# Optimization experiments

Measured on AMD Instinct MI355X. Metric: run time of the kernel, lower is better.

The kernel has to match this reference:

```python
import jax, jax.numpy as jnp
import numpy as np
import math

HEADS = 16
D_MODEL = 1024
D_K = D_MODEL // HEADS


def setup_inputs() -> dict:
    key = jax.random.key(0)
    ks = jax.random.split(key, 11)
    B, S = 2, 2048
    s = 1.0 / math.sqrt(D_MODEL)
    return {
        "q": jax.random.normal(ks[0], (B, S, D_MODEL), jnp.float32),
        "k": jax.random.normal(ks[1], (B, S, D_MODEL), jnp.float32),
        "v": jax.random.normal(ks[2], (B, S, D_MODEL), jnp.float32),
        "Wq": jax.random.normal(ks[3], (D_MODEL, D_MODEL), jnp.float32) * s,
        "bq": jax.random.normal(ks[4], (D_MODEL,), jnp.float32) * s,
        "Wk": jax.random.normal(ks[5], (D_MODEL, D_MODEL), jnp.float32) * s,
        "bk": jax.random.normal(ks[6], (D_MODEL,), jnp.float32) * s,
        "Wv": jax.random.normal(ks[7], (D_MODEL, D_MODEL), jnp.float32) * s,
        "bv": jax.random.normal(ks[8], (D_MODEL,), jnp.float32) * s,
        "Wo": jax.random.normal(ks[9], (D_MODEL, D_MODEL), jnp.float32) * s,
        "bo": jax.random.normal(ks[10], (D_MODEL,), jnp.float32) * s,
    }


def reference(q, k, v, Wq, bq, Wk, bk, Wv, bv, Wo, bo):
    B, S, _ = q.shape
    # linear projections, split heads: [B, H, S, d_k]
    def proj(x, W, b):
        y = x @ W.T + b
        return y.reshape(B, -1, HEADS, D_K).transpose(0, 2, 1, 3)
    qh, kh, vh = proj(q, Wq, bq), proj(k, Wk, bk), proj(v, Wv, bv)
    # abs-modified scaled dot-product attention (no mask, eval -> no dropout)
    scores = jnp.abs(jnp.einsum("bhsd,bhtd->bhst", qh, kh) / math.sqrt(D_K))
    attn = jax.nn.softmax(scores, axis=-1)
    out = jnp.einsum("bhst,bhtd->bhsd", attn, vh)
    concat = out.transpose(0, 2, 1, 3).reshape(B, S, D_MODEL)
    return concat @ Wo.T + bo
```

## Files before the change

### kernel.cpp

```cpp
#include <hip/hip_runtime.h>

#define HEADS 16
#define DK 64
#define DM 1024
#define SEQ 2048
#define BATCH 2

using bf16x8 = __attribute__((ext_vector_type(8))) short;
using short4v = __attribute__((ext_vector_type(4))) short;
using f32x4 = __attribute__((ext_vector_type(4))) float;

static __device__ __forceinline__ short f2bf(float x) {
  union { float f; unsigned u; } c;
  c.f = x;
  unsigned r = (c.u + 0x7FFFu + ((c.u >> 16) & 1u)) >> 16;
  return (short)r;
}

static __device__ __forceinline__ unsigned pk2bf(float lo, float hi) {
#if __has_builtin(__builtin_amdgcn_cvt_pk_bf16_f32)
  auto t = __builtin_amdgcn_cvt_pk_bf16_f32(lo, hi);
  if constexpr (sizeof(t) == 4) {
    unsigned u;
    __builtin_memcpy(&u, &t, 4);
    return u;
  } else {
    return (unsigned)(unsigned short)f2bf(lo) |
           ((unsigned)(unsigned short)f2bf(hi) << 16);
  }
#else
  return (unsigned)(unsigned short)f2bf(lo) |
         ((unsigned)(unsigned short)f2bf(hi) << 16);
#endif
}

static __device__ __forceinline__ void gload_lds16(const void* g, void* l) {
  __builtin_amdgcn_global_load_lds(
      (const __attribute__((address_space(1))) void*)g,
      (__attribute__((address_space(3))) void*)l, 16, 0, 0);
}

__global__ __launch_bounds__(256) void cvt7(
    const float* __restrict__ s0, const float* __restrict__ s1,
    const float* __restrict__ s2, const float* __restrict__ s3,
    const float* __restrict__ s4, const float* __restrict__ s5,
    const float* __restrict__ s6, short* d0, short* d1, short* d2, short* d3,
    short* d4, short* d5, short* d6) {
  const int y = blockIdx.y;
  const float* s;
  short* d;
  int n;
  switch (y) {
    case 0: s = s0; d = d0; n = BATCH * SEQ * DM; break;
    case 1: s = s1; d = d1; n = BATCH * SEQ * DM; break;
    case 2: s = s2; d = d2; n = BATCH * SEQ * DM; break;
    case 3: s = s3; d = d3; n = DM * DM; break;
    case 4: s = s4; d = d4; n = DM * DM; break;
    case 5: s = s5; d = d5; n = DM * DM; break;
    default: s = s6; d = d6; n = DM * DM; break;
  }
  const int n4 = n >> 2;
  const int stride = gridDim.x * 256;
  for (int i = blockIdx.x * 256 + threadIdx.x; i < n4; i += stride) {
    float4 v = ((const float4*)s)[i];
    uint2 o;
    o.x = pk2bf(v.x, v.y);
    o.y = pk2bf(v.z, v.w);
    ((uint2*)d)[i] = o;
  }
}

__global__ __launch_bounds__(256) void proj_qkv(
    const short* __restrict__ Aq, const short* __restrict__ Ak,
    const short* __restrict__ Av, const short* __restrict__ Wq_,
    const short* __restrict__ Wk_, const short* __restrict__ Wv_,
    const float* __restrict__ bq, const float* __restrict__ bk,
    const float* __restrict__ bv, short* __restrict__ Qh,
    short* __restrict__ Kh, short* __restrict__ Vt) {
  __shared__ short smem[128 * 136];
  short* As = smem;
  short* Ws = smem + 8192;

  const int z = blockIdx.z;
  const short* A = z == 0 ? Aq : z == 1 ? Ak : Av;
  const short* W = z == 0 ? Wq_ : z == 1 ? Wk_ : Wv_;
  const float* bias = z == 0 ? bq : z == 1 ? bk : bv;
  short* C = z == 0 ? Qh : z == 1 ? Kh : Vt;
  const bool tr = (z == 2);

  const int tid = threadIdx.x;
  const int wave = tid >> 6, lane = tid & 63;
  const int quad = lane >> 4, l15 = lane & 15;
  const int n0 = blockIdx.x * 128, m0 = blockIdx.y * 128;
  const int mh = (wave & 1) * 64, nh = (wave >> 1) * 64;
  const int ldr = lane >> 3, ldc = lane & 7;

  f32x4 acc[4][4] = {};

  for (int k0 = 0; k0 < 1024; k0 += 64) {
    __syncthreads();
#pragma unroll
    for (int i = 0; i < 8; ++i) {
      int seg = wave * 8 + i;
      int r = (seg & 15) * 8 + ldr;
      int kb = ldc ^ (r & 7);
      if (seg < 16)
        gload_lds16(&A[(size_t)(m0 + r) * 1024 + k0 + kb * 8], &As[seg * 512]);
      else
        gload_lds16(&W[(size_t)(n0 + r) * 1024 + k0 + kb * 8],
                    &Ws[(seg - 16) * 512]);
    }
    __syncthreads();
#pragma unroll
    for (int ks = 0; ks < 2; ++ks) {
      bf16x8 a[4], b[4];
      int kb = ks * 4 + quad;
#pragma unroll
      for (int f = 0; f < 4; ++f) {
        int rm = mh + f * 16 + l15;
        int rn = nh + f * 16 + l15;
        a[f] = *(const bf16x8*)&As[rm * 64 + (kb ^ (rm & 7)) * 8];
        b[f] = *(const bf16x8*)&Ws[rn * 64 + (kb ^ (rn & 7)) * 8];
      }
#pragma unroll
      for (int mf = 0; mf < 4; ++mf)
#pragma unroll
        for (int nf = 0; nf < 4; ++nf)
          acc[mf][nf] = __builtin_amdgcn_mfma_f32_16x16x32_bf16(
              a[mf], b[nf], acc[mf][nf], 0, 0, 0);
    }
  }

  float bvv[4];
#pragma unroll
  for (int nf = 0; nf < 4; ++nf) bvv[nf] = bias[n0 + nh + nf * 16 + l15];

  __syncthreads();
  short* Cb = smem;

  if (!tr) {
#pragma unroll
    for (int mf = 0; mf < 4; ++mf)
#pragma unroll
      for (int r = 0; r < 4; ++r) {
        int row = mh + mf * 16 + quad * 4 + r;
        unsigned u01 =
            pk2bf(acc[mf][0][r] + bvv[0], acc[mf][1][r] + bvv[1]);
        unsigned u23 =
            pk2bf(acc[mf][2][r] + bvv[2], acc[mf][3][r] + bvv[3]);
        Cb[row * 136 + nh + l15] = (short)u01;
        Cb[row * 136 + nh + 16 + l15] = (short)(u01 >> 16);
        Cb[row * 136 + nh + 32 + l15] = (short)u23;
        Cb[row * 136 + nh + 48 + l15] = (short)(u23 >> 16);
      }
    __syncthreads();
#pragma unroll
    for (int j = 0; j < 8; ++j) {
      int cid = tid + 256 * j;
      int row = cid >> 4, cb = cid & 15;
      bf16x8 v = *(const bf16x8*)&Cb[row * 136 + cb * 8];
      int m = m0 + row, n = n0 + cb * 8;
      int b = m >> 11, s = m & (SEQ - 1), h = n >> 6, d = n & 63;
      *(bf16x8*)&C[((size_t)(b * HEADS + h) * SEQ + s) * DK + d] = v;
    }
  } else {
#pragma unroll
    for (int mf = 0; mf < 4; ++mf)
#pragma unroll
      for (int nf = 0; nf < 4; ++nf) {
        unsigned u01 =
            pk2bf(acc[mf][nf][0] + bvv[nf], acc[mf][nf][1] + bvv[nf]);
        unsigned u23 =
            pk2bf(acc[mf][nf][2] + bvv[nf], acc[mf][nf][3] + bvv[nf]);
        int base_ = (nh + nf * 16 + l15) * 136 + mh + mf * 16 + quad * 4;
        *(unsigned*)&Cb[base_] = u01;
        *(unsigned*)&Cb[base_ + 2] = u23;
      }
    __syncthreads();
#pragma unroll
    for (int j = 0; j < 8; ++j) {
      int cid = tid + 256 * j;
      int row = cid >> 4, cb = cid & 15;
      bf16x8 v = *(const bf16x8*)&Cb[row * 136 + cb * 8];
      int n = n0 + row, m = m0 + cb * 8;
      int b = m >> 11, s = m & (SEQ - 1), h = n >> 6, d = n & 63;
      *(bf16x8*)&C[((size_t)(b * HEADS + h) * DK + d) * SEQ + s] = v;
    }
  }
}

__global__ __launch_bounds__(256) void proj_out(const short* __restrict__ A,
                                                const short* __restrict__ W,
                                                const float* __restrict__ bias,
                                                float* __restrict__ C) {
  __shared__ short smem[12288];
  short* As = smem;
  short* Ws = smem + 8192;

  const int tid = threadIdx.x;
  const int wave = tid >> 6, lane = tid & 63;
  const int quad = lane >> 4, l15 = lane & 15;
  const int n0 = blockIdx.x * 64, m0 = blockIdx.y * 128;
  const int mh = (wave & 1) * 64, nh = (wave >> 1) * 32;
  const int ldr = lane >> 3, ldc = lane & 7;

  f32x4 acc[4][2] = {};

  for (int k0 = 0; k0 < 1024; k0 += 64) {
    __syncthreads();
#pragma unroll
    for (int i = 0; i < 6; ++i) {
      int seg = wave * 6 + i;
      if (seg < 16) {
        int r = seg * 8 + ldr;
        int kb = ldc ^ (r & 7);
        gload_lds16(&A[(size_t)(m0 + r) * 1024 + k0 + kb * 8], &As[seg * 512]);
      } else {
        int r = (seg - 16) * 8 + ldr;
        int kb = ldc ^ (r & 7);
        gload_lds16(&W[(size_t)(n0 + r) * 1024 + k0 + kb * 8],
                    &Ws[(seg - 16) * 512]);
      }
    }
    __syncthreads();
#pragma unroll
    for (int ks = 0; ks < 2; ++ks) {
      bf16x8 a[4], b[2];
      int kb = ks * 4 + quad;
#pragma unroll
      for (int f = 0; f < 4; ++f) {
        int rm = mh + f * 16 + l15;
        a[f] = *(const bf16x8*)&As[rm * 64 + (kb ^ (rm & 7)) * 8];
      }
#pragma unroll
      for (int f = 0; f < 2; ++f) {
        int rn = nh + f * 16 + l15;
        b[f] = *(const bf16x8*)&Ws[rn * 64 + (kb ^ (rn & 7)) * 8];
      }
#pragma unroll
      for (int mf = 0; mf < 4; ++mf)
#pragma unroll
        for (int nf = 0; nf < 2; ++nf)
          acc[mf][nf] = __builtin_amdgcn_mfma_f32_16x16x32_bf16(
              a[mf], b[nf], acc[mf][nf], 0, 0, 0);
    }
  }

  float bvv[2];
#pragma unroll
  for (int nf = 0; nf < 2; ++nf) bvv[nf] = bias[n0 + nh + nf * 16 + l15];
#pragma unroll
  for (int mf = 0; mf < 4; ++mf)
#pragma unroll
    for (int nf = 0; nf < 2; ++nf)
#pragma unroll
      for (int r = 0; r < 4; ++r)
        C[(size_t)(m0 + mh + mf * 16 + quad * 4 + r) * 1024 + n0 + nh +
          nf * 16 + l15] = acc[mf][nf][r] + bvv[nf];
}

__global__ __launch_bounds__(128) void attn_mfma(const short* __restrict__ Qh,
                                                 const short* __restrict__ Kh,
                                                 const short* __restrict__ VtG,
                                                 short* __restrict__ concat) {
  __shared__ short Ks[2][64 * 64];
  __shared__ short Vt[2][64 * 64];
  __shared__ short Ps[64 * 64];

  const int tid = threadIdx.x;
  const int wave = tid >> 6, lane = tid & 63;
  const int quad = lane >> 4, l15 = lane & 15;
  const int bh = blockIdx.y;
  const int q0 = blockIdx.x * 64;
  const size_t base = (size_t)bh * SEQ * DK;
  const int ldr = lane >> 3, ldc = lane & 7;

  bf16x8 qf[2][2];
#pragma unroll
  for (int mf = 0; mf < 2; ++mf)
#pragma unroll
    for (int ks = 0; ks < 2; ++ks)
      qf[mf][ks] =
          *(const bf16x8*)&Qh[base +
                              (size_t)(q0 + wave * 32 + mf * 16 + l15) * 64 +
                              ks * 32 + quad * 8];

  f32x4 O[2][4] = {};
  float lsum[2][4] = {};

#define STAGE_TILE(kt_, buf_)                                              \
  {                                                                        \
    _Pragma("unroll") for (int i_ = 0; i_ < 4; ++i_) {                     \
      int seg = wave * 4 + i_;                                             \
      int row = seg * 8 + ldr;                                             \
      int kb = ldc ^ (row & 7);                                            \
      int key = 2 * (row & 15) + ((row >> 4) & 1) + 32 * (row >> 5);       \
      gload_lds16(&Kh[base + (size_t)((kt_)*64 + key) * 64 + kb * 8],      \
                  &Ks[buf_][seg * 512]);                                   \
      gload_lds16(&VtG[base + (size_t)row * SEQ + (kt_)*64 + kb * 8],      \
                  &Vt[buf_][seg * 512]);                                   \
    }                                                                      \
  }

  STAGE_TILE(0, 0);

  const float CE = 0.18033688011112042f;

  for (int kt = 0; kt < SEQ / 64; ++kt) {
    const int cur = kt & 1;
    __syncthreads();
    if (kt + 1 < SEQ / 64) STAGE_TILE(kt + 1, cur ^ 1);

    f32x4 sf[2][4] = {};
#pragma unroll
    for (int ks = 0; ks < 2; ++ks) {
      bf16x8 bfr[4];
      int kb = ks * 4 + quad;
#pragma unroll
      for (int nf = 0; nf < 4; ++nf) {
        int n = nf * 16 + l15;
        bfr[nf] = *(const bf16x8*)&Ks[cur][n * 64 + (kb ^ (n & 7)) * 8];
      }
#pragma unroll
      for (int mf = 0; mf < 2; ++mf)
#pragma unroll
        for (int nf = 0; nf < 4; ++nf)
          sf[mf][nf] = __builtin_amdgcn_mfma_f32_16x16x32_bf16(
              qf[mf][ks], bfr[nf], sf[mf][nf], 0, 0, 0);
    }

#pragma unroll
    for (int mf = 0; mf < 2; ++mf)
#pragma unroll
      for (int r = 0; r < 4; ++r) {
        float e0 = exp2f(fabsf(sf[mf][0][r]) * CE);
        float e1 = exp2f(fabsf(sf[mf][1][r]) * CE);
        float e2 = exp2f(fabsf(sf[mf][2][r]) * CE);
        float e3 = exp2f(fabsf(sf[mf][3][r]) * CE);
        lsum[mf][r] += (e0 + e1) + (e2 + e3);
        unsigned u01 = pk2bf(e0, e1);
        unsigned u23 = pk2bf(e2, e3);
        int row = wave * 32 + mf * 16 + quad * 4 + r;
        int sw = (row >> 1) & 7;
        int off = (2 * l15) & 7;
        short* rp = &Ps[row * 64];
        *(unsigned*)&rp[(((l15 >> 2) ^ sw) << 3) + off] = u01;
        *(unsigned*)&rp[(((4 + (l15 >> 2)) ^ sw) << 3) + off] = u23;
      }
    __threadfence_block();

#pragma unroll
    for (int ks = 0; ks < 2; ++ks) {
      bf16x8 av[2], bvv[4];
      int kb = ks * 4 + quad;
#pragma unroll
      for (int mf = 0; mf < 2; ++mf) {
        int row = wave * 32 + mf * 16 + l15;
        av[mf] =
            *(const bf16x8*)&Ps[row * 64 + ((kb ^ ((row >> 1) & 7)) << 3)];
      }
#pragma unroll
      for (int nf = 0; nf < 4; ++nf) {
        int n = nf * 16 + l15;
        bvv[nf] = *(const bf16x8*)&Vt[cur][n * 64 + (kb ^ (n & 7)) * 8];
      }
#pragma unroll
      for (int mf = 0; mf < 2; ++mf)
#pragma unroll
        for (int nf = 0; nf < 4; ++nf)
          O[mf][nf] = __builtin_amdgcn_mfma_f32_16x16x32_bf16(
              av[mf], bvv[nf], O[mf][nf], 0, 0, 0);
    }
  }

  float inv[2][4];
#pragma unroll
  for (int mf = 0; mf < 2; ++mf)
#pragma unroll
    for (int r = 0; r < 4; ++r) {
      float s = lsum[mf][r];
#pragma unroll
      for (int x = 1; x < 16; x <<= 1) s += __shfl_xor(s, x, 64);
      inv[mf][r] = 1.f / s;
    }

  __syncthreads();
#pragma unroll
  for (int mf = 0; mf < 2; ++mf)
#pragma unroll
    for (int r = 0; r < 4; ++r) {
      unsigned u01 =
          pk2bf(O[mf][0][r] * inv[mf][r], O[mf][1][r] * inv[mf][r]);
      unsigned u23 =
          pk2bf(O[mf][2][r] * inv[mf][r], O[mf][3][r] * inv[mf][r]);
      int row = wave * 32 + mf * 16 + quad * 4 + r;
      int sw = (row >> 1) & 7;
      short* rp = &Ps[row * 64];
      rp[((((l15) >> 3) ^ sw) << 3) + (l15 & 7)] = (short)u01;
      rp[((((16 + l15) >> 3) ^ sw) << 3) + (l15 & 7)] = (short)(u01 >> 16);
      rp[((((32 + l15) >> 3) ^ sw) << 3) + (l15 & 7)] = (short)u23;
      rp[((((48 + l15) >> 3) ^ sw) << 3) + (l15 & 7)] = (short)(u23 >> 16);
    }
  __syncthreads();
  const int b = bh >> 4, h = bh & 15;
#pragma unroll
  for (int j = 0; j < 4; ++j) {
    int cid = tid + 128 * j;
    int row = cid >> 3, cb = cid & 7;
    bf16x8 v = *(const bf16x8*)&Ps[row * 64 + ((cb ^ ((row >> 1) & 7)) << 3)];
    *(bf16x8*)&concat[((size_t)(b * SEQ + q0 + row)) * DM + h * 64 + cb * 8] =
        v;
  }
#undef STAGE_TILE
}

extern "C" void kernel_launch(void* const* d_in, const int* in_sizes, int n_in,
                              void* d_out, int out_size, void* d_ws,
                              size_t ws_size, hipStream_t stream) {
  const float* q = (const float*)d_in[0];
  const float* k = (const float*)d_in[1];
  const float* v = (const float*)d_in[2];
  const float* Wq = (const float*)d_in[3];
  const float* bq = (const float*)d_in[4];
  const float* Wk = (const float*)d_in[5];
  const float* bk = (const float*)d_in[6];
  const float* Wv = (const float*)d_in[7];
  const float* bv = (const float*)d_in[8];
  const float* Wo = (const float*)d_in[9];
  const float* bo = (const float*)d_in[10];

  short* ws = (short*)d_ws;
  const size_t T4 = (size_t)BATCH * SEQ * DM;
  const size_t T1 = (size_t)DM * DM;
  short* qb = ws;
  short* kb_ = ws + T4;
  short* vb = ws + 2 * T4;
  short* Wqb = ws + 3 * T4;
  short* Wkb = Wqb + T1;
  short* Wvb = Wqb + 2 * T1;
  short* Wob = Wqb + 3 * T1;
  short* Qh = Wqb + 4 * T1;
  short* Kh = Qh + T4;
  short* VtG = Qh + 2 * T4;
  short* cc = Qh + 3 * T4;

  cvt7<<<dim3(1024, 7), 256, 0, stream>>>(q, k, v, Wq, Wk, Wv, Wo, qb, kb_, vb,
                                          Wqb, Wkb, Wvb, Wob);

  proj_qkv<<<dim3(DM / 128, (BATCH * SEQ) / 128, 3), 256, 0, stream>>>(
      qb, kb_, vb, Wqb, Wkb, Wvb, bq, bk, bv, Qh, Kh, VtG);

  attn_mfma<<<dim3(SEQ / 64, BATCH * HEADS), 128, 0, stream>>>(Qh, Kh, VtG,
                                                               cc);

  proj_out<<<dim3(DM / 64, (BATCH * SEQ) / 128), 256, 0, stream>>>(
      cc, Wob, bo, (float*)d_out);
}
```

Before: 266.7 us.

## Split attention block into four 16-row waves and drop K/V double buffering

```diff
diff --git a/kernel.cpp b/kernel.cpp
--- a/kernel.cpp
+++ b/kernel.cpp
@@ -259,12 +259,12 @@
           nf * 16 + l15] = acc[mf][nf][r] + bvv[nf];
 }
 
-__global__ __launch_bounds__(128) void attn_mfma(const short* __restrict__ Qh,
+__global__ __launch_bounds__(256) void attn_mfma(const short* __restrict__ Qh,
                                                  const short* __restrict__ Kh,
                                                  const short* __restrict__ VtG,
                                                  short* __restrict__ concat) {
-  __shared__ short Ks[2][64 * 64];
-  __shared__ short Vt[2][64 * 64];
+  __shared__ short Ks[64 * 64];
+  __shared__ short Vt[64 * 64];
   __shared__ short Ps[64 * 64];
 
   const int tid = threadIdx.x;
@@ -275,43 +275,32 @@
   const size_t base = (size_t)bh * SEQ * DK;
   const int ldr = lane >> 3, ldc = lane & 7;
 
-  bf16x8 qf[2][2];
-#pragma unroll
-  for (int mf = 0; mf < 2; ++mf)
-#pragma unroll
-    for (int ks = 0; ks < 2; ++ks)
-      qf[mf][ks] =
-          *(const bf16x8*)&Qh[base +
-                              (size_t)(q0 + wave * 32 + mf * 16 + l15) * 64 +
-                              ks * 32 + quad * 8];
-
-  f32x4 O[2][4] = {};
-  float lsum[2][4] = {};
-
-#define STAGE_TILE(kt_, buf_)                                              \
-  {                                                                        \
-    _Pragma("unroll") for (int i_ = 0; i_ < 4; ++i_) {                     \
-      int seg = wave * 4 + i_;                                             \
-      int row = seg * 8 + ldr;                                             \
-      int kb = ldc ^ (row & 7);                                            \
-      int key = 2 * (row & 15) + ((row >> 4) & 1) + 32 * (row >> 5);       \
-      gload_lds16(&Kh[base + (size_t)((kt_)*64 + key) * 64 + kb * 8],      \
-                  &Ks[buf_][seg * 512]);                                   \
-      gload_lds16(&VtG[base + (size_t)row * SEQ + (kt_)*64 + kb * 8],      \
-                  &Vt[buf_][seg * 512]);                                   \
-    }                                                                      \
-  }
-
-  STAGE_TILE(0, 0);
+  bf16x8 qf[2];
+#pragma unroll
+  for (int ks = 0; ks < 2; ++ks)
+    qf[ks] = *(const bf16x8*)&Qh[base + (size_t)(q0 + wave * 16 + l15) * 64 +
+                                 ks * 32 + quad * 8];
+
+  f32x4 O[4] = {};
+  float lsum[4] = {};
 
   const float CE = 0.18033688011112042f;
 
   for (int kt = 0; kt < SEQ / 64; ++kt) {
-    const int cur = kt & 1;
-    __syncthreads();
-    if (kt + 1 < SEQ / 64) STAGE_TILE(kt + 1, cur ^ 1);
-
-    f32x4 sf[2][4] = {};
+    __syncthreads();
+#pragma unroll
+    for (int i = 0; i < 2; ++i) {
+      int seg = wave * 2 + i;
+      int row = seg * 8 + ldr;
+      int kb = ldc ^ (row & 7);
+      gload_lds16(&Kh[base + (size_t)(kt * 64 + row) * 64 + kb * 8],
+                  &Ks[seg * 512]);
+      gload_lds16(&VtG[base + (size_t)row * SEQ + kt * 64 + kb * 8],
+                  &Vt[seg * 512]);
+    }
+    __syncthreads();
+
+    f32x4 sf[4] = {};
 #pragma unroll
     for (int ks = 0; ks < 2; ++ks) {
       bf16x8 bfr[4];
@@ -319,99 +308,85 @@
 #pragma unroll
       for (int nf = 0; nf < 4; ++nf) {
         int n = nf * 16 + l15;
-        bfr[nf] = *(const bf16x8*)&Ks[cur][n * 64 + (kb ^ (n & 7)) * 8];
-      }
-#pragma unroll
-      for (int mf = 0; mf < 2; ++mf)
-#pragma unroll
-        for (int nf = 0; nf < 4; ++nf)
-          sf[mf][nf] = __builtin_amdgcn_mfma_f32_16x16x32_bf16(
-              qf[mf][ks], bfr[nf], sf[mf][nf], 0, 0, 0);
-    }
-
-#pragma unroll
-    for (int mf = 0; mf < 2; ++mf)
-#pragma unroll
-      for (int r = 0; r < 4; ++r) {
-        float e0 = exp2f(fabsf(sf[mf][0][r]) * CE);
-        float e1 = exp2f(fabsf(sf[mf][1][r]) * CE);
-        float e2 = exp2f(fabsf(sf[mf][2][r]) * CE);
-        float e3 = exp2f(fabsf(sf[mf][3][r]) * CE);
-        lsum[mf][r] += (e0 + e1) + (e2 + e3);
-        unsigned u01 = pk2bf(e0, e1);
-        unsigned u23 = pk2bf(e2, e3);
-        int row = wave * 32 + mf * 16 + quad * 4 + r;
-        int sw = (row >> 1) & 7;
-        int off = (2 * l15) & 7;
-        short* rp = &Ps[row * 64];
-        *(unsigned*)&rp[(((l15 >> 2) ^ sw) << 3) + off] = u01;
-        *(unsigned*)&rp[(((4 + (l15 >> 2)) ^ sw) << 3) + off] = u23;
-      }
+        bfr[nf] = *(const bf16x8*)&Ks[n * 64 + (kb ^ (n & 7)) * 8];
+      }
+#pragma unroll
+      for (int nf = 0; nf < 4; ++nf)
+        sf[nf] = __builtin_amdgcn_mfma_f32_16x16x32_bf16(qf[ks], bfr[nf],
+                                                         sf[nf], 0, 0, 0);
+    }
+
+    const int h2 = l15 >> 3, lo3 = l15 & 7;
+#pragma unroll
+    for (int r = 0; r < 4; ++r) {
+      float e0 = exp2f(fabsf(sf[0][r]) * CE);
+      float e1 = exp2f(fabsf(sf[1][r]) * CE);
+      float e2 = exp2f(fabsf(sf[2][r]) * CE);
+      float e3 = exp2f(fabsf(sf[3][r]) * CE);
+      lsum[r] += (e0 + e1) + (e2 + e3);
+      unsigned u01 = pk2bf(e0, e1);
+      unsigned u23 = pk2bf(e2, e3);
+      int row = wave * 16 + quad * 4 + r;
+      int sw = (row >> 1) & 7;
+      short* rp = &Ps[row * 64];
+      rp[(((0 + h2) ^ sw) << 3) + lo3] = (short)u01;
+      rp[(((2 + h2) ^ sw) << 3) + lo3] = (short)(u01 >> 16);
+      rp[(((4 + h2) ^ sw) << 3) + lo3] = (short)u23;
+      rp[(((6 + h2) ^ sw) << 3) + lo3] = (short)(u23 >> 16);
+    }
     __threadfence_block();
 
 #pragma unroll
     for (int ks = 0; ks < 2; ++ks) {
-      bf16x8 av[2], bvv[4];
+      bf16x8 av, bvv[4];
       int kb = ks * 4 + quad;
-#pragma unroll
-      for (int mf = 0; mf < 2; ++mf) {
-        int row = wave * 32 + mf * 16 + l15;
-        av[mf] =
-            *(const bf16x8*)&Ps[row * 64 + ((kb ^ ((row >> 1) & 7)) << 3)];
-      }
+      int row = wave * 16 + l15;
+      av = *(const bf16x8*)&Ps[row * 64 + ((kb ^ ((row >> 1) & 7)) << 3)];
 #pragma unroll
       for (int nf = 0; nf < 4; ++nf) {
         int n = nf * 16 + l15;
-        bvv[nf] = *(const bf16x8*)&Vt[cur][n * 64 + (kb ^ (n & 7)) * 8];
-      }
-#pragma unroll
-      for (int mf = 0; mf < 2; ++mf)
-#pragma unroll
-        for (int nf = 0; nf < 4; ++nf)
-          O[mf][nf] = __builtin_amdgcn_mfma_f32_16x16x32_bf16(
-              av[mf], bvv[nf], O[mf][nf], 0, 0, 0);
-    }
-  }
-
-  float inv[2][4];
-#pragma unroll
-  for (int mf = 0; mf < 2; ++mf)
-#pragma unroll
-    for (int r = 0; r < 4; ++r) {
-      float s = lsum[mf][r];
-#pragma unroll
-      for (int x = 1; x < 16; x <<= 1) s += __shfl_xor(s, x, 64);
-      inv[mf][r] = 1.f / s;
-    }
+        bvv[nf] = *(const bf16x8*)&Vt[n * 64 + (kb ^ (n & 7)) * 8];
+      }
+#pragma unroll
+      for (int nf = 0; nf < 4; ++nf)
+        O[nf] = __builtin_amdgcn_mfma_f32_16x16x32_bf16(av, bvv[nf], O[nf], 0,
+                                                        0, 0);
+    }
+  }
+
+  float inv[4];
+#pragma unroll
+  for (int r = 0; r < 4; ++r) {
+    float s = lsum[r];
+#pragma unroll
+    for (int x = 1; x < 16; x <<= 1) s += __shfl_xor(s, x, 64);
+    inv[r] = 1.f / s;
+  }
 
   __syncthreads();
-#pragma unroll
-  for (int mf = 0; mf < 2; ++mf)
-#pragma unroll
-    for (int r = 0; r < 4; ++r) {
-      unsigned u01 =
-          pk2bf(O[mf][0][r] * inv[mf][r], O[mf][1][r] * inv[mf][r]);
-      unsigned u23 =
-          pk2bf(O[mf][2][r] * inv[mf][r], O[mf][3][r] * inv[mf][r]);
-      int row = wave * 32 + mf * 16 + quad * 4 + r;
-      int sw = (row >> 1) & 7;
-      short* rp = &Ps[row * 64];
-      rp[((((l15) >> 3) ^ sw) << 3) + (l15 & 7)] = (short)u01;
-      rp[((((16 + l15) >> 3) ^ sw) << 3) + (l15 & 7)] = (short)(u01 >> 16);
-      rp[((((32 + l15) >> 3) ^ sw) << 3) + (l15 & 7)] = (short)u23;
-      rp[((((48 + l15) >> 3) ^ sw) << 3) + (l15 & 7)] = (short)(u23 >> 16);
-    }
+  const int h2 = l15 >> 3, lo3 = l15 & 7;
+#pragma unroll
+  for (int r = 0; r < 4; ++r) {
+    unsigned u01 = pk2bf(O[0][r] * inv[r], O[1][r] * inv[r]);
+    unsigned u23 = pk2bf(O[2][r] * inv[r], O[3][r] * inv[r]);
+    int row = wave * 16 + quad * 4 + r;
+    int sw = (row >> 1) & 7;
+    short* rp = &Ps[row * 64];
+    rp[(((0 + h2) ^ sw) << 3) + lo3] = (short)u01;
+    rp[(((2 + h2) ^ sw) << 3) + lo3] = (short)(u01 >> 16);
+    rp[(((4 + h2) ^ sw) << 3) + lo3] = (short)u23;
+    rp[(((6 + h2) ^ sw) << 3) + lo3] = (short)(u23 >> 16);
+  }
   __syncthreads();
   const int b = bh >> 4, h = bh & 15;
 #pragma unroll
-  for (int j = 0; j < 4; ++j) {
-    int cid = tid + 128 * j;
+  for (int j = 0; j < 2; ++j) {
+    int cid = tid + 256 * j;
     int row = cid >> 3, cb = cid & 7;
     bf16x8 v = *(const bf16x8*)&Ps[row * 64 + ((cb ^ ((row >> 1) & 7)) << 3)];
     *(bf16x8*)&concat[((size_t)(b * SEQ + q0 + row)) * DM + h * 64 + cb * 8] =
         v;
   }
-#undef STAGE_TILE
 }
 
 extern "C" void kernel_launch(void* const* d_in, const int* in_sizes, int n_in,
@@ -450,7 +425,7 @@
   proj_qkv<<<dim3(DM / 128, (BATCH * SEQ) / 128, 3), 256, 0, stream>>>(
       qb, kb_, vb, Wqb, Wkb, Wvb, bq, bk, bv, Qh, Kh, VtG);
 
-  attn_mfma<<<dim3(SEQ / 64, BATCH * HEADS), 128, 0, stream>>>(Qh, Kh, VtG,
+  attn_mfma<<<dim3(SEQ / 64, BATCH * HEADS), 256, 0, stream>>>(Qh, Kh, VtG,
                                                                cc);
 
   proj_out<<<dim3(DM / 64, (BATCH * SEQ) / 128), 256, 0, stream>>>(
```

Result: faster. 254.8 us (-4.4%).

## Double query rows per attention block and reorder V-transpose/P layouts

Applied to the files above, without the earlier changes.

```diff
diff --git a/kernel.cpp b/kernel.cpp
--- a/kernel.cpp
+++ b/kernel.cpp
@@ -167,15 +167,13 @@
 #pragma unroll
     for (int mf = 0; mf < 4; ++mf)
 #pragma unroll
-      for (int nf = 0; nf < 4; ++nf) {
-        unsigned u01 =
-            pk2bf(acc[mf][nf][0] + bvv[nf], acc[mf][nf][1] + bvv[nf]);
-        unsigned u23 =
-            pk2bf(acc[mf][nf][2] + bvv[nf], acc[mf][nf][3] + bvv[nf]);
-        int base_ = (nh + nf * 16 + l15) * 136 + mh + mf * 16 + quad * 4;
-        *(unsigned*)&Cb[base_] = u01;
-        *(unsigned*)&Cb[base_ + 2] = u23;
-      }
+      for (int nf = 0; nf < 4; ++nf)
+#pragma unroll
+        for (int j = 0; j < 4; ++j) {
+          int slot = 16 * quad + 4 * j + mf;
+          Cb[(nh + nf * 16 + l15) * 136 + mh + slot] =
+              f2bf(acc[mf][nf][j] + bvv[nf]);
+        }
     __syncthreads();
 #pragma unroll
     for (int j = 0; j < 8; ++j) {
@@ -259,59 +257,57 @@
           nf * 16 + l15] = acc[mf][nf][r] + bvv[nf];
 }
 
-__global__ __launch_bounds__(128) void attn_mfma(const short* __restrict__ Qh,
-                                                 const short* __restrict__ Kh,
-                                                 const short* __restrict__ VtG,
-                                                 short* __restrict__ concat) {
+__global__ __launch_bounds__(128, 1) void attn_mfma(
+    const short* __restrict__ Qh, const short* __restrict__ Kh,
+    const short* __restrict__ VtG, short* __restrict__ concat) {
   __shared__ short Ks[2][64 * 64];
   __shared__ short Vt[2][64 * 64];
-  __shared__ short Ps[64 * 64];
+  __shared__ short Ps[128 * 64];
 
   const int tid = threadIdx.x;
   const int wave = tid >> 6, lane = tid & 63;
   const int quad = lane >> 4, l15 = lane & 15;
   const int bh = blockIdx.y;
-  const int q0 = blockIdx.x * 64;
+  const int q0 = blockIdx.x * 128;
   const size_t base = (size_t)bh * SEQ * DK;
   const int ldr = lane >> 3, ldc = lane & 7;
 
-  bf16x8 qf[2][2];
-#pragma unroll
-  for (int mf = 0; mf < 2; ++mf)
+  bf16x8 qf[4][2];
+#pragma unroll
+  for (int mf = 0; mf < 4; ++mf)
 #pragma unroll
     for (int ks = 0; ks < 2; ++ks)
       qf[mf][ks] =
           *(const bf16x8*)&Qh[base +
-                              (size_t)(q0 + wave * 32 + mf * 16 + l15) * 64 +
+                              (size_t)(q0 + wave * 64 + mf * 16 + l15) * 64 +
                               ks * 32 + quad * 8];
 
-  f32x4 O[2][4] = {};
-  float lsum[2][4] = {};
-
-#define STAGE_TILE(kt_, buf_)                                              \
-  {                                                                        \
-    _Pragma("unroll") for (int i_ = 0; i_ < 4; ++i_) {                     \
-      int seg = wave * 4 + i_;                                             \
-      int row = seg * 8 + ldr;                                             \
-      int kb = ldc ^ (row & 7);                                            \
-      int key = 2 * (row & 15) + ((row >> 4) & 1) + 32 * (row >> 5);       \
-      gload_lds16(&Kh[base + (size_t)((kt_)*64 + key) * 64 + kb * 8],      \
-                  &Ks[buf_][seg * 512]);                                   \
-      gload_lds16(&VtG[base + (size_t)row * SEQ + (kt_)*64 + kb * 8],      \
-                  &Vt[buf_][seg * 512]);                                   \
-    }                                                                      \
+  f32x4 O[4][4] = {};
+  float lsum[4][4] = {};
+
+  const float CE = 0.18033688011112042f;
+
+#define STAGE_TILE(kt_, b_)                                               \
+  {                                                                       \
+    _Pragma("unroll") for (int i_ = 0; i_ < 4; ++i_) {                    \
+      int seg = wave * 4 + i_;                                            \
+      int row = seg * 8 + ldr;                                            \
+      int kb = ldc ^ (row & 7);                                           \
+      gload_lds16(&Kh[base + (size_t)((kt_)*64 + row) * 64 + kb * 8],     \
+                  &Ks[b_][seg * 512]);                                    \
+      gload_lds16(&VtG[base + (size_t)row * SEQ + (kt_)*64 + kb * 8],     \
+                  &Vt[b_][seg * 512]);                                    \
+    }                                                                     \
   }
 
   STAGE_TILE(0, 0);
-
-  const float CE = 0.18033688011112042f;
 
   for (int kt = 0; kt < SEQ / 64; ++kt) {
     const int cur = kt & 1;
     __syncthreads();
     if (kt + 1 < SEQ / 64) STAGE_TILE(kt + 1, cur ^ 1);
 
-    f32x4 sf[2][4] = {};
+    f32x4 sf[4][4] = {};
 #pragma unroll
     for (int ks = 0; ks < 2; ++ks) {
       bf16x8 bfr[4];
@@ -322,7 +318,7 @@
         bfr[nf] = *(const bf16x8*)&Ks[cur][n * 64 + (kb ^ (n & 7)) * 8];
       }
 #pragma unroll
-      for (int mf = 0; mf < 2; ++mf)
+      for (int mf = 0; mf < 4; ++mf)
 #pragma unroll
         for (int nf = 0; nf < 4; ++nf)
           sf[mf][nf] = __builtin_amdgcn_mfma_f32_16x16x32_bf16(
@@ -330,7 +326,7 @@
     }
 
 #pragma unroll
-    for (int mf = 0; mf < 2; ++mf)
+    for (int mf = 0; mf < 4; ++mf)
 #pragma unroll
       for (int r = 0; r < 4; ++r) {
         float e0 = exp2f(fabsf(sf[mf][0][r]) * CE);
@@ -338,24 +334,23 @@
         float e2 = exp2f(fabsf(sf[mf][2][r]) * CE);
         float e3 = exp2f(fabsf(sf[mf][3][r]) * CE);
         lsum[mf][r] += (e0 + e1) + (e2 + e3);
-        unsigned u01 = pk2bf(e0, e1);
-        unsigned u23 = pk2bf(e2, e3);
-        int row = wave * 32 + mf * 16 + quad * 4 + r;
+        uint2 u;
+        u.x = pk2bf(e0, e1);
+        u.y = pk2bf(e2, e3);
+        int row = wave * 64 + mf * 16 + quad * 4 + r;
         int sw = (row >> 1) & 7;
-        int off = (2 * l15) & 7;
-        short* rp = &Ps[row * 64];
-        *(unsigned*)&rp[(((l15 >> 2) ^ sw) << 3) + off] = u01;
-        *(unsigned*)&rp[(((4 + (l15 >> 2)) ^ sw) << 3) + off] = u23;
+        int off = ((((l15 >> 1) ^ sw) << 3) + 4 * (l15 & 1));
+        *(uint2*)&Ps[row * 64 + off] = u;
       }
     __threadfence_block();
 
 #pragma unroll
     for (int ks = 0; ks < 2; ++ks) {
-      bf16x8 av[2], bvv[4];
+      bf16x8 av[4], bvv[4];
       int kb = ks * 4 + quad;
 #pragma unroll
-      for (int mf = 0; mf < 2; ++mf) {
-        int row = wave * 32 + mf * 16 + l15;
+      for (int mf = 0; mf < 4; ++mf) {
+        int row = wave * 64 + mf * 16 + l15;
         av[mf] =
             *(const bf16x8*)&Ps[row * 64 + ((kb ^ ((row >> 1) & 7)) << 3)];
       }
@@ -365,7 +360,7 @@
         bvv[nf] = *(const bf16x8*)&Vt[cur][n * 64 + (kb ^ (n & 7)) * 8];
       }
 #pragma unroll
-      for (int mf = 0; mf < 2; ++mf)
+      for (int mf = 0; mf < 4; ++mf)
 #pragma unroll
         for (int nf = 0; nf < 4; ++nf)
           O[mf][nf] = __builtin_amdgcn_mfma_f32_16x16x32_bf16(
@@ -373,9 +368,9 @@
     }
   }
 
-  float inv[2][4];
-#pragma unroll
-  for (int mf = 0; mf < 2; ++mf)
+  float inv[4][4];
+#pragma unroll
+  for (int mf = 0; mf < 4; ++mf)
 #pragma unroll
     for (int r = 0; r < 4; ++r) {
       float s = lsum[mf][r];
@@ -384,27 +379,25 @@
       inv[mf][r] = 1.f / s;
     }
 
-  __syncthreads();
-#pragma unroll
-  for (int mf = 0; mf < 2; ++mf)
+  const int h2 = l15 >> 3, lo3 = l15 & 7;
+#pragma unroll
+  for (int mf = 0; mf < 4; ++mf)
 #pragma unroll
     for (int r = 0; r < 4; ++r) {
-      unsigned u01 =
-          pk2bf(O[mf][0][r] * inv[mf][r], O[mf][1][r] * inv[mf][r]);
-      unsigned u23 =
-          pk2bf(O[mf][2][r] * inv[mf][r], O[mf][3][r] * inv[mf][r]);
-      int row = wave * 32 + mf * 16 + quad * 4 + r;
+      unsigned u01 = pk2bf(O[mf][0][r] * inv[mf][r], O[mf][1][r] * inv[mf][r]);
+      unsigned u23 = pk2bf(O[mf][2][r] * inv[mf][r], O[mf][3][r] * inv[mf][r]);
+      int row = wave * 64 + mf * 16 + quad * 4 + r;
       int sw = (row >> 1) & 7;
       short* rp = &Ps[row * 64];
-      rp[((((l15) >> 3) ^ sw) << 3) + (l15 & 7)] = (short)u01;
-      rp[((((16 + l15) >> 3) ^ sw) << 3) + (l15 & 7)] = (short)(u01 >> 16);
-      rp[((((32 + l15) >> 3) ^ sw) << 3) + (l15 & 7)] = (short)u23;
-      rp[((((48 + l15) >> 3) ^ sw) << 3) + (l15 & 7)] = (short)(u23 >> 16);
+      rp[(((0 + h2) ^ sw) << 3) + lo3] = (short)u01;
+      rp[(((2 + h2) ^ sw) << 3) + lo3] = (short)(u01 >> 16);
+      rp[(((4 + h2) ^ sw) << 3) + lo3] = (short)u23;
+      rp[(((6 + h2) ^ sw) << 3) + lo3] = (short)(u23 >> 16);
     }
   __syncthreads();
   const int b = bh >> 4, h = bh & 15;
 #pragma unroll
-  for (int j = 0; j < 4; ++j) {
+  for (int j = 0; j < 8; ++j) {
     int cid = tid + 128 * j;
     int row = cid >> 3, cb = cid & 7;
     bf16x8 v = *(const bf16x8*)&Ps[row * 64 + ((cb ^ ((row >> 1) & 7)) << 3)];
@@ -450,8 +443,8 @@
   proj_qkv<<<dim3(DM / 128, (BATCH * SEQ) / 128, 3), 256, 0, stream>>>(
       qb, kb_, vb, Wqb, Wkb, Wvb, bq, bk, bv, Qh, Kh, VtG);
 
-  attn_mfma<<<dim3(SEQ / 64, BATCH * HEADS), 128, 0, stream>>>(Qh, Kh, VtG,
-                                                               cc);
+  attn_mfma<<<dim3(SEQ / 128, BATCH * HEADS), 128, 0, stream>>>(Qh, Kh, VtG,
+                                                                cc);
 
   proj_out<<<dim3(DM / 64, (BATCH * SEQ) / 128), 256, 0, stream>>>(
       cc, Wob, bo, (float*)d_out);
```

After: 273.9 us. 1.03x slower.
